# Performance work log

Measured on AMD Instinct MI355X. Metric: run time of the kernel, lower is better.

The kernel has to match this reference:

```python
import jax, jax.numpy as jnp
import numpy as np

DN = ('NCHW', 'OIHW', 'NCHW')

def _conv(x, w, padding):
    return jax.lax.conv_general_dilated(
        x, w, window_strides=(1, 1), padding=padding,
        dimension_numbers=DN)

def setup_inputs() -> dict:
    key = jax.random.key(0)
    k1, k2, k3, k4, k5 = jax.random.split(key, 5)
    nf = 40
    x = jax.random.normal(k1, (16, nf, 256, 256), dtype=jnp.float32)
    # PyTorch conv default init scale ~ 1/sqrt(fan_in)
    w2 = jax.random.normal(k2, (nf, nf, 1, 1), dtype=jnp.float32) / np.sqrt(nf)
    b2 = jax.random.normal(k3, (nf,), dtype=jnp.float32) * 0.01
    w3 = jax.random.normal(k4, (nf, nf, 3, 3), dtype=jnp.float32) / np.sqrt(nf * 9)
    w4 = jax.random.normal(k5, (nf, nf, 3, 3), dtype=jnp.float32) / np.sqrt(nf * 9)
    return {"x": x, "w2": w2, "b2": b2, "w3": w3, "w4": w4}

def reference(x, w2, b2, w3, w4):
    # k2: 1x1 conv + bias, then sigmoid gate (pixel attention)
    y = _conv(x, w2, padding='VALID') + b2[None, :, None, None]
    y = jax.nn.sigmoid(y)
    # k3: 3x3 conv (pad 1, no bias), gated elementwise
    out = _conv(x, w3, padding=((1, 1), (1, 1))) * y
    # k4: 3x3 conv (pad 1, no bias)
    out = _conv(out, w4, padding=((1, 1), (1, 1)))
    return out
```

## Files before the change

kernel.cpp:

```cpp
#include <hip/hip_runtime.h>
#include <hip/hip_bf16.h>

typedef __bf16 bf16;
typedef __bf16 bf16x2 __attribute__((ext_vector_type(2)));
typedef __bf16 bf16x4 __attribute__((ext_vector_type(4)));
typedef __bf16 bf16x8 __attribute__((ext_vector_type(8)));
typedef float f32x4 __attribute__((ext_vector_type(4)));

#define NF 40
#define HW 256
#define KPAD 384
#define MPAD 48

#define ZROW_ELEM_OFF (2 * MPAD * KPAD + MPAD * 64)
#define GATED_ELEM_OFF 40960
#define IMG_ELEMS ((size_t)16 * HW * HW * NF)
#define XT_ELEM_OFF (GATED_ELEM_OFF + IMG_ELEMS)
#define WS_FULL  ((GATED_ELEM_OFF + 2 * IMG_ELEMS) * 2)

#define PLANE ((size_t)HW * HW * 8)
#define IMGSTR ((size_t)HW * HW * NF)

#define SRW 34
#define SRU 340
#define SGS 2720
#define SNU 1700
#define SBUF 14336

__device__ __forceinline__ void gload_lds16(const bf16* g, bf16* l) {
  __builtin_amdgcn_global_load_lds(
      (const __attribute__((address_space(1))) void*)g,
      (__attribute__((address_space(3))) void*)l, 16, 0, 0);
}

#define BARRIER_VM(N)                                                        \
  asm volatile("s_waitcnt vmcnt(" #N ") lgkmcnt(0)\n\ts_barrier" ::: "memory")

__device__ __forceinline__ int swz_block(int bid) {
  return ((bid & 7) << 3) + ((bid >> 3) & 7) + (bid & ~63);
}

__global__ void prep_weights(const float* __restrict__ w2,
                             const float* __restrict__ w3,
                             const float* __restrict__ w4,
                             bf16* __restrict__ ws) {
  int i = blockIdx.x * 256 + threadIdx.x;
  const int T = MPAD * KPAD;
  if (i < T) {
    int co = i / KPAD, k = i % KPAD;
    float v3 = 0.f, v4 = 0.f;
    if (co < NF && k < 360) {
      int tap = k / NF, ci = k - tap * NF;
      int ky = tap / 3, kx = tap - ky * 3;
      int idx = ((co * NF + ci) * 3 + ky) * 3 + kx;
      v3 = w3[idx];
      v4 = w4[idx];
    }
    ws[i] = (bf16)v3;
    ws[T + i] = (bf16)v4;
  }
  if (i < MPAD * 64) {
    int co = i / 64, ci = i - co * 64;
    float v = 0.f;
    if (co < NF && ci < NF) v = w2[co * NF + ci];
    ws[2 * T + i] = (bf16)v;
  }
  if (i < 1024) ws[ZROW_ELEM_OFF + i] = (bf16)0.f;
}

__global__ __launch_bounds__(256, 8)
void transpose_nhwc(const float* __restrict__ x, bf16* __restrict__ xT) {
  __shared__ bf16 xs[5 * 2056];
  const int tid = threadIdx.x;
  const int row = blockIdx.x;
  const int n   = blockIdx.y;
  const size_t nb = (size_t)n * NF * HW * HW + (size_t)row * HW;

#pragma unroll
  for (int cc = 0; cc < 10; ++cc) {
    bf16x4 v;
#pragma unroll
    for (int j = 0; j < 4; ++j)
      v[j] = (bf16)x[nb + (size_t)(cc * 4 + j) * HW * HW + tid];
    *(bf16x4*)&xs[(cc >> 1) * 2056 + tid * 8 + (cc & 1) * 4] = v;
  }
  __syncthreads();

  const size_t ob = ((size_t)n * HW * HW + (size_t)row * HW) * NF;
#pragma unroll
  for (int k = 0; k < 10; ++k) {
    int u = tid + k * 256;
    int px = u / 10, c4 = u - px * 10;
    bf16x4 v = *(const bf16x4*)&xs[(c4 >> 1) * 2056 + px * 8 + (c4 & 1) * 4];
    *(bf16x4*)&xT[ob + (size_t)u * 4] = v;
  }
}

__global__ __launch_bounds__(256, 2)
void k1_sweep(const bf16* __restrict__ xT, const float* __restrict__ b2,
              const bf16* __restrict__ ws, bf16* __restrict__ gated) {
  __shared__ bf16 xs[2][SBUF];

  const int tid  = threadIdx.x;
  const int lane = tid & 63;
  const int wid  = tid >> 6;
  const int l15  = lane & 15;
  const int lk   = lane >> 4;
  const int l    = swz_block(blockIdx.x);
  const int n    = l >> 5;
  const int X0   = (l & 7) * 32;
  const int Yb   = ((l >> 3) & 3) * 64;
  const bool lasty = (Yb == HW - 64);

  const bf16* W3A  = ws;
  const bf16* W2A  = ws + 2 * MPAD * KPAD;
  const bf16* zrow = ws + ZROW_ELEM_OFF;
  const bf16* bn   = xT + (size_t)n * IMGSTR;

  int gp3[12];
#pragma unroll
  for (int kk = 0; kk < 12; ++kk) {
    int k0 = kk * 32 + lk * 8;
    int kc = (k0 < 360) ? k0 : 0;
    int tap = kc / NF, ci0 = kc - tap * NF;
    int ky = tap / 3, kx = tap - ky * 3;
    gp3[kk] = (ci0 >> 3) * SGS + (ky * SRW + kx) * 8;
  }
  int gctr[2];
#pragma unroll
  for (int kk = 0; kk < 2; ++kk) {
    int k0 = kk * 32 + lk * 8;
    int ci0 = (k0 < NF) ? k0 : 0;
    gctr[kk] = (ci0 >> 3) * SGS + (SRW + 1) * 8;
  }
  int pb[4];
#pragma unroll
  for (int q = 0; q < 4; ++q)
    pb[q] = ((wid * 2 + (q >> 1)) * SRW + (q & 1) * 16 + l15) * 8;
  float b2v[3][4];
#pragma unroll
  for (int mt = 0; mt < 3; ++mt)
#pragma unroll
    for (int r = 0; r < 4; ++r) {
      int co = mt * 16 + lk * 4 + r;
      b2v[mt][r] = (co < NF) ? b2[co] : 0.f;
    }
  bf16x8 a2[2][3];
#pragma unroll
  for (int kk = 0; kk < 2; ++kk)
#pragma unroll
    for (int mt = 0; mt < 3; ++mt)
      a2[kk][mt] = *(const bf16x8*)&W2A[(mt * 16 + l15) * 64 + kk * 32 + lk * 8];

  int ur[7], ugx[7], uc8[7], uld[7];
  bool uok[7];
#pragma unroll
  for (int it = 0; it < 7; ++it) {
    int u0 = it * 256 + wid * 64;
    int u  = u0 + lane;
    int c   = u / SRU;
    int rem = u - c * SRU;
    int r   = rem / SRW;
    int p   = rem - r * SRW;
    int gx  = X0 - 1 + p;
    uok[it] = (u < SNU) && ((unsigned)gx < HW);
    ur[it]  = r;
    ugx[it] = ((unsigned)gx < HW) ? gx : 0;
    uc8[it] = (c << 3);
    uld[it] = u0 * 8;
  }

  const bf16* P[7];
#pragma unroll
  for (int it = 0; it < 7; ++it)
    P[it] = uok[it] ? (bn + (size_t)((Yb + 7 + ur[it]) * HW + ugx[it]) * NF + uc8[it])
                    : zrow;
  const size_t PSTEP = (size_t)8 * HW * NF;

  {
    int ys = Yb - 1;
#pragma unroll
    for (int it = 0; it < 7; ++it) {
      int gy = ys + ur[it];
      bool ok = uok[it] && ((unsigned)gy < HW);
      const bf16* src = ok ? (bn + (size_t)(gy * HW + ugx[it]) * NF + uc8[it]) : zrow;
      gload_lds16(src, &xs[0][uld[it]]);
    }
  }
  asm volatile("s_waitcnt vmcnt(0) lgkmcnt(0)\n\ts_barrier" ::: "memory");

  bf16* gbase = gated + (size_t)n * IMGSTR;
  size_t e0 = ((size_t)(Yb + wid * 2) * HW + X0 + l15) * 8;
  const size_t ESTEP = (size_t)8 * HW * 8;

  for (int s = 0; s < 8; ++s) {
    const bf16* buf = xs[s & 1];

    if (s < 7) {
      bf16* nbuf = xs[(s & 1) ^ 1];
      if (lasty && s == 6) {
#pragma unroll
        for (int it = 0; it < 7; ++it) {
          bool ok = uok[it] && (ur[it] < 9);
          gload_lds16(ok ? P[it] : zrow, &nbuf[uld[it]]);
        }
      } else {
#pragma unroll
        for (int it = 0; it < 7; ++it) {
          gload_lds16(P[it], &nbuf[uld[it]]);
          P[it] += uok[it] ? PSTEP : 0;
        }
      }
    }
    asm volatile("" ::: "memory");

    bf16x4 gv[4][3];
    {
      f32x4 g[4][3];
#pragma unroll
      for (int q = 0; q < 4; ++q)
#pragma unroll
        for (int mt = 0; mt < 3; ++mt) g[q][mt] = f32x4{0, 0, 0, 0};
#pragma unroll
      for (int kk = 0; kk < 2; ++kk)
#pragma unroll
        for (int q = 0; q < 4; ++q) {
          bf16x8 b = *(const bf16x8*)&buf[gctr[kk] + pb[q]];
#pragma unroll
          for (int mt = 0; mt < 3; ++mt)
            g[q][mt] = __builtin_amdgcn_mfma_f32_16x16x32_bf16(a2[kk][mt], b, g[q][mt], 0, 0, 0);
        }
#pragma unroll
      for (int q = 0; q < 4; ++q)
#pragma unroll
        for (int mt = 0; mt < 3; ++mt)
#pragma unroll
          for (int r = 0; r < 4; ++r)
            gv[q][mt][r] = (bf16)(1.f / (1.f + __expf(-(g[q][mt][r] + b2v[mt][r]))));
    }

    f32x4 f[4][3];
#pragma unroll
    for (int q = 0; q < 4; ++q)
#pragma unroll
      for (int mt = 0; mt < 3; ++mt) f[q][mt] = f32x4{0, 0, 0, 0};

    __builtin_amdgcn_s_setprio(1);
#pragma unroll
    for (int kk = 0; kk < 12; ++kk) {
      bf16x8 a[3];
#pragma unroll
      for (int mt = 0; mt < 3; ++mt)
        a[mt] = *(const bf16x8*)&W3A[(mt * 16 + l15) * KPAD + kk * 32 + lk * 8];
#pragma unroll
      for (int q = 0; q < 4; ++q) {
        bf16x8 b = *(const bf16x8*)&buf[gp3[kk] + pb[q]];
#pragma unroll
        for (int mt = 0; mt < 3; ++mt)
          f[q][mt] = __builtin_amdgcn_mfma_f32_16x16x32_bf16(a[mt], b, f[q][mt], 0, 0, 0);
      }
    }
    __builtin_amdgcn_s_setprio(0);

#pragma unroll
    for (int q = 0; q < 4; ++q) {
      size_t pix8 = e0 + (size_t)(((q >> 1) * HW + (q & 1) * 16) * 8);
#pragma unroll
      for (int mt = 0; mt < 3; ++mt) {
        int co0 = mt * 16 + lk * 4;
        if (co0 < NF) {
          int cg = co0 >> 3;
          bf16x4 ov;
#pragma unroll
          for (int r = 0; r < 4; ++r)
            ov[r] = (bf16)(f[q][mt][r] * (float)gv[q][mt][r]);
          *(bf16x4*)&gbase[(size_t)cg * PLANE + pix8 + (co0 & 7)] = ov;
        }
      }
    }
    e0 += ESTEP;

    BARRIER_VM(12);
  }
}

__global__ __launch_bounds__(256, 2)
void k2_sweep(const bf16* __restrict__ gated, const bf16* __restrict__ ws,
              float* __restrict__ out) {
  __shared__ bf16 xs[2][SBUF];

  const int tid  = threadIdx.x;
  const int lane = tid & 63;
  const int wid  = tid >> 6;
  const int l15  = lane & 15;
  const int lk   = lane >> 4;
  const int l    = swz_block(blockIdx.x);
  const int n    = l >> 5;
  const int X0   = (l & 7) * 32;
  const int Yb   = ((l >> 3) & 3) * 64;
  const bool lasty = (Yb == HW - 64);

  const bf16* W4A  = ws + MPAD * KPAD;
  const bf16* zrow = ws + ZROW_ELEM_OFF;
  const bf16* bn   = gated + (size_t)n * IMGSTR;

  int gp4[12];
#pragma unroll
  for (int kk = 0; kk < 12; ++kk) {
    int k0 = kk * 32 + lk * 8;
    int kc = (k0 < 360) ? k0 : 0;
    int tap = kc / NF, ci0 = kc - tap * NF;
    int ky = tap / 3, kx = tap - ky * 3;
    gp4[kk] = (ci0 >> 3) * SGS + (ky * SRW + kx) * 8;
  }
  int pb[4];
#pragma unroll
  for (int q = 0; q < 4; ++q)
    pb[q] = ((wid * 2 + (q >> 1)) * SRW + (q & 1) * 16 + l15) * 8;

  int ur[7], ugx[7], ucp[7], uld[7];
  bool uok[7];
#pragma unroll
  for (int it = 0; it < 7; ++it) {
    int u0 = it * 256 + wid * 64;
    int u  = u0 + lane;
    int c   = u / SRU;
    int rem = u - c * SRU;
    int r   = rem / SRW;
    int p   = rem - r * SRW;
    int gx  = X0 - 1 + p;
    uok[it] = (u < SNU) && ((unsigned)gx < HW);
    ur[it]  = r;
    ugx[it] = ((unsigned)gx < HW) ? gx : 0;
    ucp[it] = (c < 5) ? c : 0;
    uld[it] = u0 * 8;
  }

  const bf16* P[7];
#pragma unroll
  for (int it = 0; it < 7; ++it)
    P[it] = uok[it] ? (bn + (size_t)ucp[it] * PLANE +
                       (size_t)((Yb + 7 + ur[it]) * HW + ugx[it]) * 8)
                    : zrow;
  const size_t PSTEP = (size_t)8 * HW * 8;

  {
    int ys = Yb - 1;
#pragma unroll
    for (int it = 0; it < 7; ++it) {
      int gy = ys + ur[it];
      bool ok = uok[it] && ((unsigned)gy < HW);
      const bf16* src = ok ? (bn + (size_t)ucp[it] * PLANE + (size_t)(gy * HW + ugx[it]) * 8)
                           : zrow;
      gload_lds16(src, &xs[0][uld[it]]);
    }
  }
  asm volatile("s_waitcnt vmcnt(0) lgkmcnt(0)\n\ts_barrier" ::: "memory");

  float* on = out + (size_t)n * NF * HW * HW;
  size_t o0 = (size_t)(Yb + wid * 2) * HW + X0 + l15;
  const size_t OSTEP = (size_t)8 * HW;

  for (int s = 0; s < 8; ++s) {
    const bf16* buf = xs[s & 1];

    if (s < 7) {
      bf16* nbuf = xs[(s & 1) ^ 1];
      if (lasty && s == 6) {
#pragma unroll
        for (int it = 0; it < 7; ++it) {
          bool ok = uok[it] && (ur[it] < 9);
          gload_lds16(ok ? P[it] : zrow, &nbuf[uld[it]]);
        }
      } else {
#pragma unroll
        for (int it = 0; it < 7; ++it) {
          gload_lds16(P[it], &nbuf[uld[it]]);
          P[it] += uok[it] ? PSTEP : 0;
        }
      }
    }
    asm volatile("" ::: "memory");

    f32x4 f[4][3];
#pragma unroll
    for (int q = 0; q < 4; ++q)
#pragma unroll
      for (int mt = 0; mt < 3; ++mt) f[q][mt] = f32x4{0, 0, 0, 0};

    __builtin_amdgcn_s_setprio(1);
#pragma unroll
    for (int kk = 0; kk < 12; ++kk) {
      bf16x8 a[3];
#pragma unroll
      for (int mt = 0; mt < 3; ++mt)
        a[mt] = *(const bf16x8*)&W4A[(mt * 16 + l15) * KPAD + kk * 32 + lk * 8];
#pragma unroll
      for (int q = 0; q < 4; ++q) {
        bf16x8 b = *(const bf16x8*)&buf[gp4[kk] + pb[q]];
#pragma unroll
        for (int mt = 0; mt < 3; ++mt)
          f[q][mt] = __builtin_amdgcn_mfma_f32_16x16x32_bf16(a[mt], b, f[q][mt], 0, 0, 0);
      }
    }
    __builtin_amdgcn_s_setprio(0);

#pragma unroll
    for (int q = 0; q < 4; ++q) {
      float* orow = on + o0 + ((q >> 1) * HW + (q & 1) * 16);
#pragma unroll
      for (int mt = 0; mt < 3; ++mt)
#pragma unroll
        for (int r = 0; r < 4; ++r) {
          int co = mt * 16 + lk * 4 + r;
          if (co < NF)
            orow[(size_t)co * HW * HW] = f[q][mt][r];
        }
    }
    o0 += OSTEP;

    BARRIER_VM(48);
  }
}

#define K1_RW 18
__global__ __launch_bounds__(512, 6)
void k1_gate_nchw(const float* __restrict__ x, const float* __restrict__ b2,
                  const bf16* __restrict__ ws, bf16* __restrict__ gated) {
  __shared__ bf16 xs[K1_RW * K1_RW * NF];

  const int tid  = threadIdx.x;
  const int lane = tid & 63;
  const int wid  = tid >> 6;
  const int l15  = lane & 15;
  const int lk   = lane >> 4;
  const int n    = blockIdx.z;
  const int X0   = blockIdx.x * 16;
  const int Y0   = blockIdx.y * 16;

  const bf16* W3A = ws;
  const bf16* W2A = ws + 2 * MPAD * KPAD;

  const float* xn = x + (size_t)n * NF * HW * HW;
  for (int i = tid; i < K1_RW * K1_RW * NF / 2; i += 512) {
    int cih = i / (K1_RW * K1_RW);
    int rem = i - cih * (K1_RW * K1_RW);
    int ci  = cih * 2;
    int yy  = rem / K1_RW, xx = rem - yy * K1_RW;
    int gy  = Y0 - 1 + yy, gx = X0 - 1 + xx;
    float v0 = 0.f, v1 = 0.f;
    if ((unsigned)gy < HW && (unsigned)gx < HW) {
      const float* p = xn + (size_t)ci * HW * HW + gy * HW + gx;
      v0 = p[0];
      v1 = p[HW * HW];
    }
    bf16x2 pr; pr[0] = (bf16)v0; pr[1] = (bf16)v1;
    *(bf16x2*)&xs[rem * NF + ci] = pr;
  }

  int off3[12];
#pragma unroll
  for (int kk = 0; kk < 12; ++kk) {
    int k0 = kk * 32 + lk * 8;
    int kc = (k0 < 360) ? k0 : 0;
    int tap = kc / NF, ci0 = kc - tap * NF;
    int ky = tap / 3, kx = tap - ky * 3;
    off3[kk] = (ky * K1_RW + kx) * NF + ci0;
  }
  int pb[2];
#pragma unroll
  for (int t2 = 0; t2 < 2; ++t2) {
    int pix = (wid * 2 + t2) * 16 + l15;
    int py = pix >> 4, px = pix & 15;
    pb[t2] = (py * K1_RW + px) * NF;
  }
  float b2v[3][4];
#pragma unroll
  for (int mt = 0; mt < 3; ++mt)
#pragma unroll
    for (int r = 0; r < 4; ++r) {
      int co = mt * 16 + lk * 4 + r;
      b2v[mt][r] = (co < NF) ? b2[co] : 0.f;
    }

  __syncthreads();

  bf16x4 gv[2][3];
  {
    f32x4 g[2][3];
#pragma unroll
    for (int t2 = 0; t2 < 2; ++t2)
#pragma unroll
      for (int mt = 0; mt < 3; ++mt) g[t2][mt] = f32x4{0, 0, 0, 0};
#pragma unroll
    for (int kk = 0; kk < 2; ++kk) {
      int k0 = kk * 32 + lk * 8;
      int goff = (K1_RW + 1) * NF + ((k0 < NF) ? k0 : 0);
      bf16x8 a[3];
#pragma unroll
      for (int mt = 0; mt < 3; ++mt)
        a[mt] = *(const bf16x8*)&W2A[(mt * 16 + l15) * 64 + k0];
#pragma unroll
      for (int t2 = 0; t2 < 2; ++t2) {
        bf16x8 b = *(const bf16x8*)&xs[pb[t2] + goff];
#pragma unroll
        for (int mt = 0; mt < 3; ++mt)
          g[t2][mt] = __builtin_amdgcn_mfma_f32_16x16x32_bf16(a[mt], b, g[t2][mt], 0, 0, 0);
      }
    }
#pragma unroll
    for (int t2 = 0; t2 < 2; ++t2)
#pragma unroll
      for (int mt = 0; mt < 3; ++mt)
#pragma unroll
        for (int r = 0; r < 4; ++r)
          gv[t2][mt][r] = (bf16)(1.f / (1.f + __expf(-(g[t2][mt][r] + b2v[mt][r]))));
  }

  f32x4 facc[2][3];
#pragma unroll
  for (int t2 = 0; t2 < 2; ++t2)
#pragma unroll
    for (int mt = 0; mt < 3; ++mt) facc[t2][mt] = f32x4{0, 0, 0, 0};

#pragma unroll
  for (int kk = 0; kk < 12; ++kk) {
    bf16x8 a[3];
#pragma unroll
    for (int mt = 0; mt < 3; ++mt)
      a[mt] = *(const bf16x8*)&W3A[(mt * 16 + l15) * KPAD + kk * 32 + lk * 8];
#pragma unroll
    for (int t2 = 0; t2 < 2; ++t2) {
      bf16x8 b = *(const bf16x8*)&xs[pb[t2] + off3[kk]];
#pragma unroll
      for (int mt = 0; mt < 3; ++mt)
        facc[t2][mt] = __builtin_amdgcn_mfma_f32_16x16x32_bf16(a[mt], b, facc[t2][mt], 0, 0, 0);
    }
  }

#pragma unroll
  for (int t2 = 0; t2 < 2; ++t2) {
    int pix = (wid * 2 + t2) * 16 + l15;
    int py = pix >> 4, px = pix & 15;
    size_t pix8 = ((size_t)(Y0 + py) * HW + (X0 + px)) * 8;
#pragma unroll
    for (int mt = 0; mt < 3; ++mt) {
      int co0 = mt * 16 + lk * 4;
      if (co0 < NF) {
        int cg = co0 >> 3;
        bf16x4 ov;
#pragma unroll
        for (int r = 0; r < 4; ++r)
          ov[r] = (bf16)(facc[t2][mt][r] * (float)gv[t2][mt][r]);
        *(bf16x4*)&gated[(size_t)n * IMGSTR + (size_t)cg * PLANE + pix8 + (co0 & 7)] = ov;
      }
    }
  }
}

extern "C" void kernel_launch(void* const* d_in, const int* in_sizes, int n_in,
                              void* d_out, int out_size, void* d_ws, size_t ws_size,
                              hipStream_t stream) {
  const float* x  = (const float*)d_in[0];
  const float* w2 = (const float*)d_in[1];
  const float* b2 = (const float*)d_in[2];
  const float* w3 = (const float*)d_in[3];
  const float* w4 = (const float*)d_in[4];
  float* out = (float*)d_out;
  bf16* ws   = (bf16*)d_ws;

  hipLaunchKernelGGL(prep_weights, dim3(72), dim3(256), 0, stream, w2, w3, w4, ws);

  bf16* gated = ws + GATED_ELEM_OFF;
  if (ws_size >= WS_FULL) {
    bf16* xT = ws + XT_ELEM_OFF;
    hipLaunchKernelGGL(transpose_nhwc, dim3(256, 16), dim3(256), 0, stream, x, xT);
    hipLaunchKernelGGL(k1_sweep, dim3(512), dim3(256), 0, stream,
                       xT, b2, ws, gated);
  } else {
    hipLaunchKernelGGL(k1_gate_nchw, dim3(16, 16, 16), dim3(512), 0, stream,
                       x, b2, ws, gated);
  }
  hipLaunchKernelGGL(k2_sweep, dim3(512), dim3(256), 0, stream,
                     gated, ws, out);
}
```

Before: 250.9 us.

## Replace double-buffered halo tiles with an 18-row LDS ring buffer in conv sweeps

Both 3x3 conv sweep kernels now keep a ring of 18 input-row slots in LDS instead of two full 10-row tiles. Each step loads only the 8 new rows, so the 2-row halo overlap is no longer re-fetched from global memory. The ring is smaller than the two tiles, which lets launch bounds rise from 2 to 3 blocks per CU. The cost is extra per-step modular updates of the row offsets and more complex slot indexing.

```diff
diff --git a/kernel.cpp b/kernel.cpp
--- a/kernel.cpp
+++ b/kernel.cpp
@@ -21,11 +21,10 @@
 #define PLANE ((size_t)HW * HW * 8)
 #define IMGSTR ((size_t)HW * HW * NF)
 
-#define SRW 34
-#define SRU 340
-#define SGS 2720
-#define SNU 1700
-#define SBUF 14336
+#define RSLOTS 18
+#define SLOTE 1408
+#define RING_E (RSLOTS * SLOTE)
+#define SLOT_STEP (8 * SLOTE)
 
 __device__ __forceinline__ void gload_lds16(const bf16* g, bf16* l) {
   __builtin_amdgcn_global_load_lds(
@@ -96,10 +95,10 @@
   }
 }
 
-__global__ __launch_bounds__(256, 2)
+__global__ __launch_bounds__(256, 3)
 void k1_sweep(const bf16* __restrict__ xT, const float* __restrict__ b2,
               const bf16* __restrict__ ws, bf16* __restrict__ gated) {
-  __shared__ bf16 xs[2][SBUF];
+  __shared__ bf16 xs[RING_E];
 
   const int tid  = threadIdx.x;
   const int lane = tid & 63;
@@ -117,26 +116,34 @@
   const bf16* zrow = ws + ZROW_ELEM_OFF;
   const bf16* bn   = xT + (size_t)n * IMGSTR;
 
-  int gp3[12];
+  int rowoff[12][2], bnd3[12];
 #pragma unroll
   for (int kk = 0; kk < 12; ++kk) {
     int k0 = kk * 32 + lk * 8;
     int kc = (k0 < 360) ? k0 : 0;
     int tap = kc / NF, ci0 = kc - tap * NF;
     int ky = tap / 3, kx = tap - ky * 3;
-    gp3[kk] = (ci0 >> 3) * SGS + (ky * SRW + kx) * 8;
-  }
-  int gctr[2];
+    int koff = (ci0 >> 3) * 272 + kx * 8;
+    bnd3[kk] = RING_E + koff;
+#pragma unroll
+    for (int h = 0; h < 2; ++h)
+      rowoff[kk][h] = (wid * 2 + h + ky) * SLOTE + koff;
+  }
+  int grow[2][2], bndg[2];
 #pragma unroll
   for (int kk = 0; kk < 2; ++kk) {
     int k0 = kk * 32 + lk * 8;
     int ci0 = (k0 < NF) ? k0 : 0;
-    gctr[kk] = (ci0 >> 3) * SGS + (SRW + 1) * 8;
-  }
-  int pb[4];
+    int koffg = (ci0 >> 3) * 272 + 8;
+    bndg[kk] = RING_E + koffg;
+#pragma unroll
+    for (int h = 0; h < 2; ++h)
+      grow[kk][h] = (wid * 2 + h + 1) * SLOTE + koffg;
+  }
+  int cpb[4];
 #pragma unroll
   for (int q = 0; q < 4; ++q)
-    pb[q] = ((wid * 2 + (q >> 1)) * SRW + (q & 1) * 16 + l15) * 8;
+    cpb[q] = ((q & 1) * 16 + l15) * 8;
   float b2v[3][4];
 #pragma unroll
   for (int mt = 0; mt < 3; ++mt)
@@ -152,39 +159,46 @@
     for (int mt = 0; mt < 3; ++mt)
       a2[kk][mt] = *(const bf16x8*)&W2A[(mt * 16 + l15) * 64 + kk * 32 + lk * 8];
 
-  int ur[7], ugx[7], uc8[7], uld[7];
-  bool uok[7];
-#pragma unroll
-  for (int it = 0; it < 7; ++it) {
-    int u0 = it * 256 + wid * 64;
-    int u  = u0 + lane;
-    int c   = u / SRU;
-    int rem = u - c * SRU;
-    int r   = rem / SRW;
-    int p   = rem - r * SRW;
+  int ugx[6], uc8[6];
+  bool uok[6], uok7[6];
+#pragma unroll
+  for (int it = 0; it < 6; ++it) {
+    int seg = it % 3;
+    int sl2 = it / 3;
+    int u   = seg * 64 + lane;
+    int cg  = u / 34;
+    int p   = u - cg * 34;
     int gx  = X0 - 1 + p;
-    uok[it] = (u < SNU) && ((unsigned)gx < HW);
-    ur[it]  = r;
-    ugx[it] = ((unsigned)gx < HW) ? gx : 0;
-    uc8[it] = (c << 3);
-    uld[it] = u0 * 8;
-  }
-
-  const bf16* P[7];
-#pragma unroll
-  for (int it = 0; it < 7; ++it)
-    P[it] = uok[it] ? (bn + (size_t)((Yb + 7 + ur[it]) * HW + ugx[it]) * NF + uc8[it])
+    bool act = (u < 170);
+    uok[it]  = act && ((unsigned)gx < HW);
+    uok7[it] = uok[it] && ((wid * 2 + sl2) < 7);
+    ugx[it]  = ((unsigned)gx < HW) ? gx : 0;
+    uc8[it]  = (cg < 5) ? (cg << 3) : 0;
+  }
+  const bf16* P[6];
+#pragma unroll
+  for (int it = 0; it < 6; ++it) {
+    int rb = wid * 2 + (it / 3);
+    P[it] = uok[it] ? (bn + (size_t)((Yb + 9 + rb) * HW + ugx[it]) * NF + uc8[it])
                     : zrow;
+  }
   const size_t PSTEP = (size_t)8 * HW * NF;
-
-  {
-    int ys = Yb - 1;
-#pragma unroll
-    for (int it = 0; it < 7; ++it) {
-      int gy = ys + ur[it];
-      bool ok = uok[it] && ((unsigned)gy < HW);
-      const bf16* src = ok ? (bn + (size_t)(gy * HW + ugx[it]) * NF + uc8[it]) : zrow;
-      gload_lds16(src, &xs[0][uld[it]]);
+  int slotv[2] = {10 + wid * 2, 11 + wid * 2};
+
+#pragma unroll
+  for (int t = 0; t < 8; ++t) {
+    int idx = wid + 4 * t;
+    if (idx < 30) {
+      int rel = idx / 3, seg = idx - rel * 3;
+      int u = seg * 64 + lane;
+      int cg = u / 34;
+      int p  = u - cg * 34;
+      int gy = Yb - 1 + rel, gx = X0 - 1 + p;
+      bool ok = (u < 170) && ((unsigned)gy < HW) && ((unsigned)gx < HW);
+      const bf16* src = ok ? (bn + (size_t)(gy * HW + gx) * NF + ((cg < 5 ? cg : 0) << 3))
+                           : zrow;
+      if (u < 170)
+        gload_lds16(src, &xs[rel * SLOTE + seg * 512]);
     }
   }
   asm volatile("s_waitcnt vmcnt(0) lgkmcnt(0)\n\ts_barrier" ::: "memory");
@@ -194,20 +208,22 @@
   const size_t ESTEP = (size_t)8 * HW * 8;
 
   for (int s = 0; s < 8; ++s) {
-    const bf16* buf = xs[s & 1];
-
     if (s < 7) {
-      bf16* nbuf = xs[(s & 1) ^ 1];
       if (lasty && s == 6) {
 #pragma unroll
-        for (int it = 0; it < 7; ++it) {
-          bool ok = uok[it] && (ur[it] < 9);
-          gload_lds16(ok ? P[it] : zrow, &nbuf[uld[it]]);
+        for (int it = 0; it < 6; ++it) {
+          int seg = it % 3, sl2 = it / 3;
+          bf16* dst = &xs[slotv[sl2] * SLOTE + seg * 512];
+          if (seg < 2 || lane < 42)
+            gload_lds16(uok7[it] ? P[it] : zrow, dst);
         }
       } else {
 #pragma unroll
-        for (int it = 0; it < 7; ++it) {
-          gload_lds16(P[it], &nbuf[uld[it]]);
+        for (int it = 0; it < 6; ++it) {
+          int seg = it % 3, sl2 = it / 3;
+          bf16* dst = &xs[slotv[sl2] * SLOTE + seg * 512];
+          if (seg < 2 || lane < 42)
+            gload_lds16(P[it], dst);
           P[it] += uok[it] ? PSTEP : 0;
         }
       }
@@ -225,7 +241,7 @@
       for (int kk = 0; kk < 2; ++kk)
 #pragma unroll
         for (int q = 0; q < 4; ++q) {
-          bf16x8 b = *(const bf16x8*)&buf[gctr[kk] + pb[q]];
+          bf16x8 b = *(const bf16x8*)&xs[grow[kk][q >> 1] + cpb[q]];
 #pragma unroll
           for (int mt = 0; mt < 3; ++mt)
             g[q][mt] = __builtin_amdgcn_mfma_f32_16x16x32_bf16(a2[kk][mt], b, g[q][mt], 0, 0, 0);
@@ -254,7 +270,7 @@
         a[mt] = *(const bf16x8*)&W3A[(mt * 16 + l15) * KPAD + kk * 32 + lk * 8];
 #pragma unroll
       for (int q = 0; q < 4; ++q) {
-        bf16x8 b = *(const bf16x8*)&buf[gp3[kk] + pb[q]];
+        bf16x8 b = *(const bf16x8*)&xs[rowoff[kk][q >> 1] + cpb[q]];
 #pragma unroll
         for (int mt = 0; mt < 3; ++mt)
           f[q][mt] = __builtin_amdgcn_mfma_f32_16x16x32_bf16(a[mt], b, f[q][mt], 0, 0, 0);
@@ -281,13 +297,33 @@
     e0 += ESTEP;
 
     BARRIER_VM(12);
-  }
-}
-
-__global__ __launch_bounds__(256, 2)
+
+#pragma unroll
+    for (int kk = 0; kk < 12; ++kk)
+#pragma unroll
+      for (int h = 0; h < 2; ++h) {
+        rowoff[kk][h] += SLOT_STEP;
+        if (rowoff[kk][h] >= bnd3[kk]) rowoff[kk][h] -= RING_E;
+      }
+#pragma unroll
+    for (int kk = 0; kk < 2; ++kk)
+#pragma unroll
+      for (int h = 0; h < 2; ++h) {
+        grow[kk][h] += SLOT_STEP;
+        if (grow[kk][h] >= bndg[kk]) grow[kk][h] -= RING_E;
+      }
+#pragma unroll
+    for (int j = 0; j < 2; ++j) {
+      slotv[j] += 8;
+      if (slotv[j] >= RSLOTS) slotv[j] -= RSLOTS;
+    }
+  }
+}
+
+__global__ __launch_bounds__(256, 3)
 void k2_sweep(const bf16* __restrict__ gated, const bf16* __restrict__ ws,
               float* __restrict__ out) {
-  __shared__ bf16 xs[2][SBUF];
+  __shared__ bf16 xs[RING_E];
 
   const int tid  = threadIdx.x;
   const int lane = tid & 63;
@@ -304,55 +340,66 @@
   const bf16* zrow = ws + ZROW_ELEM_OFF;
   const bf16* bn   = gated + (size_t)n * IMGSTR;
 
-  int gp4[12];
+  int rowoff[12][2], bnd4[12];
 #pragma unroll
   for (int kk = 0; kk < 12; ++kk) {
     int k0 = kk * 32 + lk * 8;
     int kc = (k0 < 360) ? k0 : 0;
     int tap = kc / NF, ci0 = kc - tap * NF;
     int ky = tap / 3, kx = tap - ky * 3;
-    gp4[kk] = (ci0 >> 3) * SGS + (ky * SRW + kx) * 8;
-  }
-  int pb[4];
+    int koff = (ci0 >> 3) * 272 + kx * 8;
+    bnd4[kk] = RING_E + koff;
+#pragma unroll
+    for (int h = 0; h < 2; ++h)
+      rowoff[kk][h] = (wid * 2 + h + ky) * SLOTE + koff;
+  }
+  int cpb[4];
 #pragma unroll
   for (int q = 0; q < 4; ++q)
-    pb[q] = ((wid * 2 + (q >> 1)) * SRW + (q & 1) * 16 + l15) * 8;
-
-  int ur[7], ugx[7], ucp[7], uld[7];
-  bool uok[7];
-#pragma unroll
-  for (int it = 0; it < 7; ++it) {
-    int u0 = it * 256 + wid * 64;
-    int u  = u0 + lane;
-    int c   = u / SRU;
-    int rem = u - c * SRU;
-    int r   = rem / SRW;
-    int p   = rem - r * SRW;
+    cpb[q] = ((q & 1) * 16 + l15) * 8;
+
+  int ugx[6], ucp[6];
+  bool uok[6], uok7[6];
+#pragma unroll
+  for (int it = 0; it < 6; ++it) {
+    int seg = it % 3;
+    int sl2 = it / 3;
+    int u   = seg * 64 + lane;
+    int cg  = u / 34;
+    int p   = u - cg * 34;
     int gx  = X0 - 1 + p;
-    uok[it] = (u < SNU) && ((unsigned)gx < HW);
-    ur[it]  = r;
-    ugx[it] = ((unsigned)gx < HW) ? gx : 0;
-    ucp[it] = (c < 5) ? c : 0;
-    uld[it] = u0 * 8;
-  }
-
-  const bf16* P[7];
-#pragma unroll
-  for (int it = 0; it < 7; ++it)
+    bool act = (u < 170);
+    uok[it]  = act && ((unsigned)gx < HW);
+    uok7[it] = uok[it] && ((wid * 2 + sl2) < 7);
+    ugx[it]  = ((unsigned)gx < HW) ? gx : 0;
+    ucp[it]  = (cg < 5) ? cg : 0;
+  }
+  const bf16* P[6];
+#pragma unroll
+  for (int it = 0; it < 6; ++it) {
+    int rb = wid * 2 + (it / 3);
     P[it] = uok[it] ? (bn + (size_t)ucp[it] * PLANE +
-                       (size_t)((Yb + 7 + ur[it]) * HW + ugx[it]) * 8)
+                       (size_t)((Yb + 9 + rb) * HW + ugx[it]) * 8)
                     : zrow;
+  }
   const size_t PSTEP = (size_t)8 * HW * 8;
-
-  {
-    int ys = Yb - 1;
-#pragma unroll
-    for (int it = 0; it < 7; ++it) {
-      int gy = ys + ur[it];
-      bool ok = uok[it] && ((unsigned)gy < HW);
-      const bf16* src = ok ? (bn + (size_t)ucp[it] * PLANE + (size_t)(gy * HW + ugx[it]) * 8)
+  int slotv[2] = {10 + wid * 2, 11 + wid * 2};
+
+#pragma unroll
+  for (int t = 0; t < 8; ++t) {
+    int idx = wid + 4 * t;
+    if (idx < 30) {
+      int rel = idx / 3, seg = idx - rel * 3;
+      int u = seg * 64 + lane;
+      int cg = u / 34;
+      int p  = u - cg * 34;
+      int gy = Yb - 1 + rel, gx = X0 - 1 + p;
+      bool ok = (u < 170) && ((unsigned)gy < HW) && ((unsigned)gx < HW);
+      const bf16* src = ok ? (bn + (size_t)(cg < 5 ? cg : 0) * PLANE +
+                              (size_t)(gy * HW + gx) * 8)
                            : zrow;
-      gload_lds16(src, &xs[0][uld[it]]);
+      if (u < 170)
+        gload_lds16(src, &xs[rel * SLOTE + seg * 512]);
     }
   }
   asm volatile("s_waitcnt vmcnt(0) lgkmcnt(0)\n\ts_barrier" ::: "memory");
@@ -362,20 +409,22 @@
   const size_t OSTEP = (size_t)8 * HW;
 
   for (int s = 0; s < 8; ++s) {
-    const bf16* buf = xs[s & 1];
-
     if (s < 7) {
-      bf16* nbuf = xs[(s & 1) ^ 1];
       if (lasty && s == 6) {
 #pragma unroll
-        for (int it = 0; it < 7; ++it) {
-          bool ok = uok[it] && (ur[it] < 9);
-          gload_lds16(ok ? P[it] : zrow, &nbuf[uld[it]]);
+        for (int it = 0; it < 6; ++it) {
+          int seg = it % 3, sl2 = it / 3;
+          bf16* dst = &xs[slotv[sl2] * SLOTE + seg * 512];
+          if (seg < 2 || lane < 42)
+            gload_lds16(uok7[it] ? P[it] : zrow, dst);
         }
       } else {
 #pragma unroll
-        for (int it = 0; it < 7; ++it) {
-          gload_lds16(P[it], &nbuf[uld[it]]);
+        for (int it = 0; it < 6; ++it) {
+          int seg = it % 3, sl2 = it / 3;
+          bf16* dst = &xs[slotv[sl2] * SLOTE + seg * 512];
+          if (seg < 2 || lane < 42)
+            gload_lds16(P[it], dst);
           P[it] += uok[it] ? PSTEP : 0;
         }
       }
@@ -397,7 +446,7 @@
         a[mt] = *(const bf16x8*)&W4A[(mt * 16 + l15) * KPAD + kk * 32 + lk * 8];
 #pragma unroll
       for (int q = 0; q < 4; ++q) {
-        bf16x8 b = *(const bf16x8*)&buf[gp4[kk] + pb[q]];
+        bf16x8 b = *(const bf16x8*)&xs[rowoff[kk][q >> 1] + cpb[q]];
 #pragma unroll
         for (int mt = 0; mt < 3; ++mt)
           f[q][mt] = __builtin_amdgcn_mfma_f32_16x16x32_bf16(a[mt], b, f[q][mt], 0, 0, 0);
@@ -420,6 +469,19 @@
     o0 += OSTEP;
 
     BARRIER_VM(48);
+
+#pragma unroll
+    for (int kk = 0; kk < 12; ++kk)
+#pragma unroll
+      for (int h = 0; h < 2; ++h) {
+        rowoff[kk][h] += SLOT_STEP;
+        if (rowoff[kk][h] >= bnd4[kk]) rowoff[kk][h] -= RING_E;
+      }
+#pragma unroll
+    for (int j = 0; j < 2; ++j) {
+      slotv[j] += 8;
+      if (slotv[j] >= RSLOTS) slotv[j] -= RSLOTS;
+    }
   }
 }
 
```

Result: slower. 406.4 us (+62.0%).
